# Optimization experiments

Measured on AMD Instinct MI355X. Metric: run time of the kernel, lower is better.

Reference implementation:

```python
import jax, jax.numpy as jnp
import numpy as np

DIM = 768
NUM_HEADS = 8
HEAD_DIM = DIM // NUM_HEADS


def setup_inputs() -> dict:
    key = jax.random.key(0)
    ks = jax.random.split(key, 5)
    B, N, C = 16, 4096, DIM
    x = jax.random.normal(ks[0], (B, N, C), dtype=jnp.float32)
    # nn.Linear(dim, dim*3): weight [3C, C], bias [3C]
    w_qkv = jax.random.normal(ks[1], (3 * C, C), dtype=jnp.float32) * (C ** -0.5)
    b_qkv = jax.random.normal(ks[2], (3 * C,), dtype=jnp.float32) * 0.02
    w_proj = jax.random.normal(ks[3], (C, C), dtype=jnp.float32) * (C ** -0.5)
    b_proj = jax.random.normal(ks[4], (C,), dtype=jnp.float32) * 0.02
    return {"x": x, "w_qkv": w_qkv, "b_qkv": b_qkv, "w_proj": w_proj, "b_proj": b_proj}


def reference(x, w_qkv, b_qkv, w_proj, b_proj):
    B, N, C = x.shape
    H, D = NUM_HEADS, C // NUM_HEADS
    # qkv projection: [B,N,3C] -> [3,B,H,N,D]
    qkv = x @ w_qkv.T + b_qkv
    qkv = qkv.reshape(B, N, 3, H, D).transpose(2, 0, 3, 1, 4)
    q, k, v = qkv[0], qkv[1], qkv[2]
    # dynamic_scale=True: scale by N^-0.5
    q = q * (N ** -0.5)
    # channel attention: contract over tokens N -> [B,H,D,D]
    attn = jnp.einsum("bhnd,bhne->bhde", q, k)
    attn = jax.nn.softmax(attn, axis=-1)
    # (attn @ v^T)^T -> [B,H,N,D]
    out = jnp.einsum("bhde,bhne->bhnd", attn, v)
    out = out.transpose(0, 2, 1, 3).reshape(B, N, C)
    return out @ w_proj.T + b_proj
```

## Files before the change

### kernel.cpp

```cpp
#include <hip/hip_runtime.h>
#include <hip/hip_bf16.h>
#include <stdint.h>

typedef __bf16 bf16;
typedef __bf16 bf16x8 __attribute__((ext_vector_type(8)));
typedef __bf16 bf16x4 __attribute__((ext_vector_type(4)));
typedef float f32x4 __attribute__((ext_vector_type(4)));

__device__ __forceinline__ void gl_lds16(const bf16* g, bf16* l) {
  __builtin_amdgcn_global_load_lds(
      (const __attribute__((address_space(1))) void*)g,
      (__attribute__((address_space(3))) void*)l, 16, 0, 0);
}

__global__ void cvt_f32_bf16(const float* __restrict__ in, bf16* __restrict__ out, int n4) {
  int i = blockIdx.x * blockDim.x + threadIdx.x;
  if (i < n4) {
    float4 v = ((const float4*)in)[i];
    bf16x4 o;
    o[0] = (bf16)v.x; o[1] = (bf16)v.y; o[2] = (bf16)v.z; o[3] = (bf16)v.w;
    ((bf16x4*)out)[i] = o;
  }
}

template<int EPI>
__global__ __launch_bounds__(256) void gemm_bt(
    const bf16* __restrict__ A, const bf16* __restrict__ B,
    const float* __restrict__ bias, void* __restrict__ Cout,
    int M, int N, int K, int nbn)
{
  __shared__ __align__(16) bf16 sA[128 * 32];
  __shared__ __align__(16) bf16 sB[128 * 32];
  int bm = blockIdx.x / nbn, bn = blockIdx.x % nbn;
  int m0 = bm * 128, n0 = bn * 128;
  int t = threadIdx.x;
  int wave = t >> 6, lane = t & 63;
  int wm = wave >> 1, wn = wave & 1;
  int l16 = lane & 15, quad = lane >> 4;

  f32x4 acc[4][4] = {};

  int rA = (wave * 2) * 16 + (lane >> 2);
  int kk = (lane & 3) * 8;
  const bf16* gA = A + (long)(m0 + rA) * K + kk;
  const bf16* gB = B + (long)(n0 + rA) * K + kk;

  for (int k0 = 0; k0 < K; k0 += 32) {
    gl_lds16(gA + k0,            &sA[(wave * 2) * 512]);
    gl_lds16(gA + 16 * K + k0,   &sA[(wave * 2 + 1) * 512]);
    gl_lds16(gB + k0,            &sB[(wave * 2) * 512]);
    gl_lds16(gB + 16 * K + k0,   &sB[(wave * 2 + 1) * 512]);
    __syncthreads();
    bf16x8 af[4], bfr[4];
#pragma unroll
    for (int mi = 0; mi < 4; mi++)
      af[mi] = *(const bf16x8*)&sA[(wm * 64 + mi * 16 + l16) * 32 + quad * 8];
#pragma unroll
    for (int ni = 0; ni < 4; ni++)
      bfr[ni] = *(const bf16x8*)&sB[(wn * 64 + ni * 16 + l16) * 32 + quad * 8];
#pragma unroll
    for (int mi = 0; mi < 4; mi++)
#pragma unroll
      for (int ni = 0; ni < 4; ni++)
        acc[mi][ni] = __builtin_amdgcn_mfma_f32_16x16x32_bf16(af[mi], bfr[ni], acc[mi][ni], 0, 0, 0);
    __syncthreads();
  }

#pragma unroll
  for (int mi = 0; mi < 4; mi++) {
    int row = m0 + wm * 64 + mi * 16 + quad * 4;
#pragma unroll
    for (int ni = 0; ni < 4; ni++) {
      int col = n0 + wn * 64 + ni * 16 + l16;
      float bv = bias[col];
#pragma unroll
      for (int r = 0; r < 4; r++) {
        float v = acc[mi][ni][r] + bv;
        if (EPI == 0) {
          if (col < 768) v *= 0.015625f;
          ((bf16*)Cout)[(long)(row + r) * N + col] = (bf16)v;
        } else {
          ((float*)Cout)[(long)(row + r) * N + col] = v;
        }
      }
    }
  }
}

__global__ __launch_bounds__(256) void attn_qk(const bf16* __restrict__ qkv, float* __restrict__ part)
{
  __shared__ __align__(16) bf16 sQ[96 * 72];
  __shared__ __align__(16) bf16 sK[96 * 72];
  int bh = blockIdx.x >> 1, kb = blockIdx.x & 1;
  int b = bh >> 3, h = bh & 7;
  int t = threadIdx.x;
  int wave = t >> 6, lane = t & 63;
  int wm = wave >> 1, wn = wave & 1;
  int l16 = lane & 15, quad = lane >> 4;
  f32x4 acc[3][3] = {};
  const bf16* Qb = qkv + (long)b * 4096 * 2304 + h * 96;
  const bf16* Kb = Qb + 768;

  for (int it = 0; it < 32; it++) {
    int tok0 = kb * 2048 + it * 64;
    __syncthreads();
#pragma unroll
    for (int i = 0; i < 3; i++) {
      int id = i * 256 + t;
      int tl = id / 12, cc = id % 12;
      uint4 q4 = *(const uint4*)(Qb + (long)(tok0 + tl) * 2304 + cc * 8);
      uint4 k4 = *(const uint4*)(Kb + (long)(tok0 + tl) * 2304 + cc * 8);
      const bf16* qe = (const bf16*)&q4;
      const bf16* ke = (const bf16*)&k4;
#pragma unroll
      for (int j = 0; j < 8; j++) {
        sQ[(cc * 8 + j) * 72 + tl] = qe[j];
        sK[(cc * 8 + j) * 72 + tl] = ke[j];
      }
    }
    __syncthreads();
#pragma unroll
    for (int ks = 0; ks < 2; ks++) {
      bf16x8 af[3], bfr[3];
#pragma unroll
      for (int mi = 0; mi < 3; mi++)
        af[mi] = *(const bf16x8*)&sQ[(wm * 48 + mi * 16 + l16) * 72 + ks * 32 + quad * 8];
#pragma unroll
      for (int ni = 0; ni < 3; ni++)
        bfr[ni] = *(const bf16x8*)&sK[(wn * 48 + ni * 16 + l16) * 72 + ks * 32 + quad * 8];
#pragma unroll
      for (int mi = 0; mi < 3; mi++)
#pragma unroll
        for (int ni = 0; ni < 3; ni++)
          acc[mi][ni] = __builtin_amdgcn_mfma_f32_16x16x32_bf16(af[mi], bfr[ni], acc[mi][ni], 0, 0, 0);
    }
  }
  float* pout = part + (long)(bh * 2 + kb) * 9216;
#pragma unroll
  for (int mi = 0; mi < 3; mi++)
#pragma unroll
    for (int ni = 0; ni < 3; ni++) {
      int row = wm * 48 + mi * 16 + quad * 4;
      int col = wn * 48 + ni * 16 + l16;
#pragma unroll
      for (int r = 0; r < 4; r++)
        pout[(row + r) * 96 + col] = acc[mi][ni][r];
    }
}

__global__ __launch_bounds__(256) void softmax_attn(const float* __restrict__ part, bf16* __restrict__ attn)
{
  __shared__ float s[96 * 97];
  int bh = blockIdx.x;
  int t = threadIdx.x;
  const float* p0 = part + (long)bh * 2 * 9216;
  const float* p1 = p0 + 9216;
  for (int e = t; e < 9216; e += 256) {
    int r = e / 96, c = e % 96;
    s[r * 97 + c] = p0[e] + p1[e];
  }
  __syncthreads();
  if (t < 96) {
    float m = -1e30f;
    for (int i = 0; i < 96; i++) m = fmaxf(m, s[t * 97 + i]);
    float sum = 0.f;
    for (int i = 0; i < 96; i++) {
      float ev = __expf(s[t * 97 + i] - m);
      s[t * 97 + i] = ev;
      sum += ev;
    }
    float inv = 1.f / sum;
    bf16* ao = attn + (long)bh * 9216 + t * 96;
    for (int i = 0; i < 96; i++) ao[i] = (bf16)(s[t * 97 + i] * inv);
  }
}

__global__ __launch_bounds__(256) void attn_v(
    const bf16* __restrict__ qkv, const bf16* __restrict__ attn, bf16* __restrict__ out2)
{
  __shared__ __align__(16) bf16 sV[128 * 96];
  __shared__ __align__(16) bf16 sAt[96 * 96];
  int bh = blockIdx.x >> 5, tb = blockIdx.x & 31;
  int b = bh >> 3, h = bh & 7;
  int tok0 = tb * 128;
  int t = threadIdx.x;
  int wave = t >> 6, lane = t & 63;
  int wm = wave >> 1, wn = wave & 1;
  int l16 = lane & 15, quad = lane >> 4;
  f32x4 acc[4][3] = {};
  const bf16* Vb = qkv + (long)b * 4096 * 2304 + 1536 + h * 96;

#pragma unroll
  for (int j = 0; j < 6; j++) {
    int c = wave * 6 + j;
    int g = c * 64 + lane;
    int tok = g / 12, cc = g % 12;
    gl_lds16(Vb + (long)(tok0 + tok) * 2304 + cc * 8, &sV[c * 512]);
  }
  for (int c = wave; c < 18; c += 4) {
    int g = c * 64 + lane;
    int d = g / 12, cc = g % 12;
    gl_lds16(attn + (long)bh * 9216 + d * 96 + cc * 8, &sAt[c * 512]);
  }
  __syncthreads();
#pragma unroll
  for (int ks = 0; ks < 3; ks++) {
    bf16x8 af[4], bfr[3];
#pragma unroll
    for (int mi = 0; mi < 4; mi++)
      af[mi] = *(const bf16x8*)&sV[(wm * 64 + mi * 16 + l16) * 96 + ks * 32 + quad * 8];
#pragma unroll
    for (int ni = 0; ni < 3; ni++)
      bfr[ni] = *(const bf16x8*)&sAt[(wn * 48 + ni * 16 + l16) * 96 + ks * 32 + quad * 8];
#pragma unroll
    for (int mi = 0; mi < 4; mi++)
#pragma unroll
      for (int ni = 0; ni < 3; ni++)
        acc[mi][ni] = __builtin_amdgcn_mfma_f32_16x16x32_bf16(af[mi], bfr[ni], acc[mi][ni], 0, 0, 0);
  }
  bf16* ob = out2 + (long)(b * 4096 + tok0) * 768 + h * 96;
#pragma unroll
  for (int mi = 0; mi < 4; mi++)
#pragma unroll
    for (int ni = 0; ni < 3; ni++) {
      int row = wm * 64 + mi * 16 + quad * 4;
      int col = wn * 48 + ni * 16 + l16;
#pragma unroll
      for (int r = 0; r < 4; r++)
        ob[(long)(row + r) * 768 + col] = (bf16)acc[mi][ni][r];
    }
}

extern "C" void kernel_launch(void* const* d_in, const int* in_sizes, int n_in,
                              void* d_out, int out_size, void* d_ws, size_t ws_size,
                              hipStream_t stream) {
  const float* x      = (const float*)d_in[0];
  const float* w_qkv  = (const float*)d_in[1];
  const float* b_qkv  = (const float*)d_in[2];
  const float* w_proj = (const float*)d_in[3];
  const float* b_proj = (const float*)d_in[4];

  char* ws = (char*)d_ws;
  bf16*  Xb     = (bf16*)ws;
  bf16*  Wqkvb  = (bf16*)(ws + 100663296);
  bf16*  Wprojb = (bf16*)(ws + 104202240);
  bf16*  qkvb   = (bf16*)(ws + 105381888);
  float* part   = (float*)(ws + 407371776);
  bf16*  attnb  = (bf16*)(ws + 416808960);
  bf16*  out2   = (bf16*)ws;

  cvt_f32_bf16<<<(12582912 + 255) / 256, 256, 0, stream>>>(x, Xb, 12582912);
  cvt_f32_bf16<<<(442368 + 255) / 256, 256, 0, stream>>>(w_qkv, Wqkvb, 442368);
  cvt_f32_bf16<<<(147456 + 255) / 256, 256, 0, stream>>>(w_proj, Wprojb, 147456);

  gemm_bt<0><<<512 * 18, 256, 0, stream>>>(Xb, Wqkvb, b_qkv, qkvb, 65536, 2304, 768, 18);
  attn_qk<<<256, 256, 0, stream>>>(qkvb, part);
  softmax_attn<<<128, 256, 0, stream>>>(part, attnb);
  attn_v<<<4096, 256, 0, stream>>>(qkvb, attnb, out2);
  gemm_bt<1><<<512 * 6, 256, 0, stream>>>(out2, Wprojb, b_proj, d_out, 65536, 768, 768, 6);
}
```

Measured before the change: 940.0 us.

## Replace GEMM with 256x256 double-buffered, swizzled, ping-pong pipelined kernel

Replaces the 128x128 single-buffered GEMM used for the QKV and output projections with a 256x256-tile, 512-thread kernel. It uses BK=64, double-buffered LDS with XOR-swizzled layout, and staged half-tile prefetches interleaved with MFMA phases. It also adds s_setprio, explicit waitcnt and barrier scheduling, and remaps workgroups across XCDs for cache locality. The aim is to hide global-load latency and raise data reuse. The cost is much larger LDS use (128KB) and register pressure, and correctness depends on the hand-tuned vmcnt counts.

```diff
diff --git a/kernel.cpp b/kernel.cpp
--- a/kernel.cpp
+++ b/kernel.cpp
@@ -23,64 +23,143 @@
   }
 }
 
+
+template<int OP, int HALF>
+__device__ __forceinline__ void stage_half(const bf16* __restrict__ G, long r0, int k0,
+                                           int K, bf16* ldsOp, int w, int lane) {
+#pragma unroll
+  for (int j = 0; j < 2; ++j) {
+    int rr8 = (w * 2 + j) * 8;
+    int rb = (OP == 0) ? ((rr8 & 63) + ((rr8 >> 6) << 7) + HALF * 64)
+                       : ((rr8 & 31) + ((rr8 >> 5) << 6) + HALF * 32);
+    int row = rb + (lane >> 3);
+    int ci = (lane & 7) ^ (row & 7);
+    gl_lds16(G + (r0 + row) * (long)K + k0 + ci * 8, ldsOp + rb * 64);
+  }
+}
+
+#define AF(buf_, mi_, ksel_) (*(const bf16x8*)&lds[buf_][0][aoff0 + (mi_) * 1024 + (ksel_)])
+#define BF(buf_, ni_, ksel_) (*(const bf16x8*)&lds[buf_][1][boff0 + (ni_) * 1024 + (ksel_)])
+#define MFMA16(a_, b_, c_) c_ = __builtin_amdgcn_mfma_f32_16x16x32_bf16(a_, b_, c_, 0, 0, 0)
+
+#define TILE(t_, buf_) do {                                                         \
+    bf16x8 af[4][2], bl[2][2], bh[2][2];                                            \
+                                   \
+    _Pragma("unroll") for (int mi = 0; mi < 4; mi++) {                              \
+      af[mi][0] = AF(buf_, mi, ks0); af[mi][1] = AF(buf_, mi, ks1); }               \
+    _Pragma("unroll") for (int ni = 0; ni < 2; ni++) {                              \
+      bl[ni][0] = BF(buf_, ni, ks0); bl[ni][1] = BF(buf_, ni, ks1); }               \
+    if ((t_) + 1 < T) stage_half<1, 0>(B, n0, ((t_) + 1) * 64, K,                   \
+                                       &lds[(buf_) ^ 1][1][0], w, lane);            \
+    __builtin_amdgcn_s_barrier();                                                   \
+    asm volatile("s_waitcnt lgkmcnt(0)" ::: "memory");                              \
+    __builtin_amdgcn_s_setprio(1);                                                  \
+    _Pragma("unroll") for (int mi = 0; mi < 4; mi++)                                \
+      _Pragma("unroll") for (int ni = 0; ni < 2; ni++) {                            \
+        MFMA16(af[mi][0], bl[ni][0], acc[mi][ni]);                                  \
+        MFMA16(af[mi][1], bl[ni][1], acc[mi][ni]); }                                \
+    __builtin_amdgcn_s_setprio(0);                                                  \
+    __builtin_amdgcn_s_barrier();                                                   \
+                                          \
+    _Pragma("unroll") for (int ni = 0; ni < 2; ni++) {                              \
+      bh[ni][0] = BF(buf_, 2 + ni, ks0); bh[ni][1] = BF(buf_, 2 + ni, ks1); }       \
+    if ((t_) + 2 < T) stage_half<0, 0>(A, m0, ((t_) + 2) * 64, K,                   \
+                                       &lds[buf_][0][0], w, lane);                  \
+    __builtin_amdgcn_s_barrier();                                                   \
+    asm volatile("s_waitcnt lgkmcnt(0)" ::: "memory");                              \
+    __builtin_amdgcn_s_setprio(1);                                                  \
+    _Pragma("unroll") for (int mi = 0; mi < 4; mi++)                                \
+      _Pragma("unroll") for (int ni = 0; ni < 2; ni++) {                            \
+        MFMA16(af[mi][0], bh[ni][0], acc[mi][2 + ni]);                              \
+        MFMA16(af[mi][1], bh[ni][1], acc[mi][2 + ni]); }                            \
+    __builtin_amdgcn_s_setprio(0);                                                  \
+    __builtin_amdgcn_s_barrier();                                                   \
+                                          \
+    _Pragma("unroll") for (int mi = 0; mi < 4; mi++) {                              \
+      af[mi][0] = AF(buf_, 4 + mi, ks0); af[mi][1] = AF(buf_, 4 + mi, ks1); }       \
+    if ((t_) + 2 < T) stage_half<1, 1>(B, n0, ((t_) + 2) * 64, K,                   \
+                                       &lds[buf_][1][0], w, lane);                  \
+    __builtin_amdgcn_s_barrier();                                                   \
+    asm volatile("s_waitcnt lgkmcnt(0)" ::: "memory");                              \
+    __builtin_amdgcn_s_setprio(1);                                                  \
+    _Pragma("unroll") for (int mi = 0; mi < 4; mi++)                                \
+      _Pragma("unroll") for (int ni = 0; ni < 2; ni++) {                            \
+        MFMA16(af[mi][0], bh[ni][0], acc[4 + mi][2 + ni]);                          \
+        MFMA16(af[mi][1], bh[ni][1], acc[4 + mi][2 + ni]); }                        \
+    __builtin_amdgcn_s_setprio(0);                                                  \
+    __builtin_amdgcn_s_barrier();                                                   \
+                             \
+    if ((t_) + 2 < T) stage_half<0, 1>(A, m0, ((t_) + 2) * 64, K,                   \
+                                       &lds[buf_][0][0], w, lane);                  \
+    if ((t_) >= T - 2) { asm volatile("s_waitcnt vmcnt(0)" ::: "memory"); }         \
+    else               { asm volatile("s_waitcnt vmcnt(6)" ::: "memory"); }         \
+    __builtin_amdgcn_s_barrier();                                                   \
+    __builtin_amdgcn_s_setprio(1);                                                  \
+    _Pragma("unroll") for (int mi = 0; mi < 4; mi++)                                \
+      _Pragma("unroll") for (int ni = 0; ni < 2; ni++) {                            \
+        MFMA16(af[mi][0], bl[ni][0], acc[4 + mi][ni]);                              \
+        MFMA16(af[mi][1], bl[ni][1], acc[4 + mi][ni]); }                            \
+    __builtin_amdgcn_s_setprio(0);                                                  \
+    __builtin_amdgcn_s_barrier();                                                   \
+  } while (0)
+
 template<int EPI>
-__global__ __launch_bounds__(256) void gemm_bt(
+__global__ __launch_bounds__(512, 2) void gemm256(
     const bf16* __restrict__ A, const bf16* __restrict__ B,
     const float* __restrict__ bias, void* __restrict__ Cout,
-    int M, int N, int K, int nbn)
+    int N, int K, int nbn, int nwg)
 {
-  __shared__ __align__(16) bf16 sA[128 * 32];
-  __shared__ __align__(16) bf16 sB[128 * 32];
-  int bm = blockIdx.x / nbn, bn = blockIdx.x % nbn;
-  int m0 = bm * 128, n0 = bn * 128;
+  __shared__ __align__(16) bf16 lds[2][2][256 * 64];
+  int bid = blockIdx.x;
+  int swz = (bid & 7) * (nwg >> 3) + (bid >> 3);
+  long m0 = (long)(swz / nbn) * 256;
+  int n0i = (swz % nbn) * 256;
+  long n0 = n0i;
   int t = threadIdx.x;
-  int wave = t >> 6, lane = t & 63;
-  int wm = wave >> 1, wn = wave & 1;
+  int w = t >> 6, lane = t & 63;
+  int wm = w >> 2, wn = w & 3;
   int l16 = lane & 15, quad = lane >> 4;
-
-  f32x4 acc[4][4] = {};
-
-  int rA = (wave * 2) * 16 + (lane >> 2);
-  int kk = (lane & 3) * 8;
-  const bf16* gA = A + (long)(m0 + rA) * K + kk;
-  const bf16* gB = B + (long)(n0 + rA) * K + kk;
-
-  for (int k0 = 0; k0 < K; k0 += 32) {
-    gl_lds16(gA + k0,            &sA[(wave * 2) * 512]);
-    gl_lds16(gA + 16 * K + k0,   &sA[(wave * 2 + 1) * 512]);
-    gl_lds16(gB + k0,            &sB[(wave * 2) * 512]);
-    gl_lds16(gB + 16 * K + k0,   &sB[(wave * 2 + 1) * 512]);
-    __syncthreads();
-    bf16x8 af[4], bfr[4];
-#pragma unroll
-    for (int mi = 0; mi < 4; mi++)
-      af[mi] = *(const bf16x8*)&sA[(wm * 64 + mi * 16 + l16) * 32 + quad * 8];
-#pragma unroll
-    for (int ni = 0; ni < 4; ni++)
-      bfr[ni] = *(const bf16x8*)&sB[(wn * 64 + ni * 16 + l16) * 32 + quad * 8];
-#pragma unroll
-    for (int mi = 0; mi < 4; mi++)
-#pragma unroll
-      for (int ni = 0; ni < 4; ni++)
-        acc[mi][ni] = __builtin_amdgcn_mfma_f32_16x16x32_bf16(af[mi], bfr[ni], acc[mi][ni], 0, 0, 0);
-    __syncthreads();
-  }
-
-#pragma unroll
-  for (int mi = 0; mi < 4; mi++) {
-    int row = m0 + wm * 64 + mi * 16 + quad * 4;
+  int s7 = l16 & 7;
+  int aoff0 = (wm * 128 + l16) * 64;
+  int boff0 = (wn * 64 + l16) * 64;
+  int ks0 = (quad ^ s7) * 8;
+  int ks1 = ((4 + quad) ^ s7) * 8;
+  const int T = K >> 6;
+
+  f32x4 acc[8][4] = {};
+
+  stage_half<0, 0>(A, m0, 0, K, &lds[0][0][0], w, lane);
+  stage_half<1, 1>(B, n0, 0, K, &lds[0][1][0], w, lane);
+  stage_half<0, 1>(A, m0, 0, K, &lds[0][0][0], w, lane);
+  stage_half<1, 0>(B, n0, 0, K, &lds[0][1][0], w, lane);
+  stage_half<0, 0>(A, m0, 64, K, &lds[1][0][0], w, lane);
+  stage_half<1, 1>(B, n0, 64, K, &lds[1][1][0], w, lane);
+  stage_half<0, 1>(A, m0, 64, K, &lds[1][0][0], w, lane);
+  asm volatile("s_waitcnt vmcnt(6)" ::: "memory");
+  __builtin_amdgcn_s_barrier();
+
+  for (int tt = 0; tt < T; tt += 2) {
+    TILE(tt, 0);
+    TILE(tt + 1, 1);
+  }
+
+  long crow0 = m0 + wm * 128 + quad * 4;
+  int ccol0 = n0i + wn * 64 + l16;
+#pragma unroll
+  for (int mi = 0; mi < 8; mi++) {
 #pragma unroll
     for (int ni = 0; ni < 4; ni++) {
-      int col = n0 + wn * 64 + ni * 16 + l16;
+      int col = ccol0 + ni * 16;
       float bv = bias[col];
 #pragma unroll
       for (int r = 0; r < 4; r++) {
         float v = acc[mi][ni][r] + bv;
+        long row = crow0 + mi * 16 + r;
         if (EPI == 0) {
           if (col < 768) v *= 0.015625f;
-          ((bf16*)Cout)[(long)(row + r) * N + col] = (bf16)v;
+          ((bf16*)Cout)[row * (long)N + col] = (bf16)v;
         } else {
-          ((float*)Cout)[(long)(row + r) * N + col] = v;
+          ((float*)Cout)[row * (long)N + col] = v;
         }
       }
     }
@@ -253,9 +332,9 @@
   cvt_f32_bf16<<<(442368 + 255) / 256, 256, 0, stream>>>(w_qkv, Wqkvb, 442368);
   cvt_f32_bf16<<<(147456 + 255) / 256, 256, 0, stream>>>(w_proj, Wprojb, 147456);
 
-  gemm_bt<0><<<512 * 18, 256, 0, stream>>>(Xb, Wqkvb, b_qkv, qkvb, 65536, 2304, 768, 18);
+  gemm256<0><<<2304, 512, 0, stream>>>(Xb, Wqkvb, b_qkv, qkvb, 2304, 768, 9, 2304);
   attn_qk<<<256, 256, 0, stream>>>(qkvb, part);
   softmax_attn<<<128, 256, 0, stream>>>(part, attnb);
   attn_v<<<4096, 256, 0, stream>>>(qkvb, attnb, out2);
-  gemm_bt<1><<<512 * 6, 256, 0, stream>>>(out2, Wprojb, b_proj, d_out, 65536, 768, 768, 6);
-}
+  gemm256<1><<<768, 512, 0, stream>>>(out2, Wprojb, b_proj, d_out, 768, 768, 3, 768);
+}
```

Measured after the change: 819.7 us. -12.8%, faster.
